# Performance work log

Measured on AMD Instinct MI355X. Metric: run time of the kernel, lower is better.

## Reference

```python
import jax, jax.numpy as jnp
import numpy as np

ORDER = 7
ALPHA = 1.0
BETA = 1.0

def _jacobi_coeffs(order, a, b):
    k1 = np.zeros(order + 1, dtype=np.float32)
    k2 = np.zeros(order + 1, dtype=np.float32)
    k3 = np.zeros(order + 1, dtype=np.float32)
    for i in range(2, order + 1):
        k1[i] = (2*i + a + b) * (2*i + a + b - 1) / (2*i * (i + a + b))
        k2[i] = (2*i + a + b - 1) * (a*a - b*b) / (2*i * (i + a + b) * (2*i + a + b - 2))
        k3[i] = (i + a - 1) * (i + b - 1) * (2*i + a + b) / (i * (i + a + b) * (2*i + a + b - 2))
    return k1, k2, k3

K1, K2, K3 = _jacobi_coeffs(ORDER, ALPHA, BETA)

def setup_inputs() -> dict:
    key = jax.random.key(0)
    kx, kc = jax.random.split(key)
    batch, input_size, output_size = 4096, 512, 512
    x = jax.random.normal(kx, (batch, input_size), dtype=jnp.float32)
    coef = jax.random.normal(kc, (output_size, input_size, ORDER + 1), dtype=jnp.float32) * 0.1
    return {"x": x, "coef": coef}

def _precompute_jacobi(x):
    # x: [B, I] -> jacobi values [B, I, order+1]
    x = jnp.tanh(x)
    p0 = jnp.ones_like(x)
    p1 = 0.5 * (ALPHA + BETA + 2.0) * x - 0.5 * (ALPHA - BETA)
    vals = [p0, p1]
    for i in range(2, ORDER + 1):
        vals.append((K1[i] * x + K2[i]) * vals[i - 1] - K3[i] * vals[i - 2])
    return jnp.stack(vals, axis=2)  # [B, I, D]

def reference(x, coef):
    jac = _precompute_jacobi(x)                 # [B, I, D]
    # sum_j over input and order dims in one contraction
    return jnp.einsum('bid,jid->bj', jac, coef)  # [B, O]
```

## Files before the change

### kernel.cpp

```cpp
#include <hip/hip_runtime.h>
#include <stdint.h>

#define BATCH 4096
#define ISZ   512
#define OSZ   512
#define KDIM  4096

#define TM 128
#define TN 128
#define BK 64
#define SPLITK 4

typedef __bf16 bf16x8 __attribute__((ext_vector_type(8)));
typedef float  f32x4  __attribute__((ext_vector_type(4)));

__device__ __forceinline__ unsigned short f2bf(float f) {
    uint32_t u = __float_as_uint(f);
    u = (u + 0x7FFFu + ((u >> 16) & 1u)) >> 16;
    return (unsigned short)u;
}

__global__ __launch_bounds__(256) void convert_bf16(
    const float* __restrict__ src, unsigned short* __restrict__ dst, int n4)
{
    int idx = blockIdx.x * 256 + threadIdx.x;
    if (idx >= n4) return;
    float4 v = reinterpret_cast<const float4*>(src)[idx];
    uint2 o;
    o.x = (uint32_t)f2bf(v.x) | ((uint32_t)f2bf(v.y) << 16);
    o.y = (uint32_t)f2bf(v.z) | ((uint32_t)f2bf(v.w) << 16);
    reinterpret_cast<uint2*>(dst)[idx] = o;
}

__global__ __launch_bounds__(256, 2) void gemm_fused(
    const float* __restrict__ X,
    const unsigned short* __restrict__ Bm,
    unsigned short* __restrict__ Cp,
    int M, int N, int K)
{
    __shared__ __align__(16) unsigned short As[2][TM * BK];
    __shared__ __align__(16) unsigned short Bs[2][TN * BK];

    const int tid  = threadIdx.x;
    const int wave = tid >> 6;
    const int lane = tid & 63;
    const int wm   = (wave >> 1) * 64;
    const int wn   = (wave & 1) * 64;

    const int    m0    = blockIdx.x * TM;
    const size_t baseB = (size_t)blockIdx.y * TN * K;
    const int kper  = K / SPLITK;
    const int kbeg  = blockIdx.z * kper;
    const int niter = kper / BK;

    f32x4 acc[4][4] = {};

    const int mrow = lane & 15;
    const int kc   = lane >> 4;

    const int xr = tid >> 1;
    const int xc = (tid & 1) * 4;

    auto stageB = [&](int k0, int buf) {
        #pragma unroll
        for (int it = 0; it < 4; ++it) {
            int s    = it * 256 + tid;
            int row  = s >> 3;
            int csrc = (s & 7) ^ (row & 7);
            const unsigned short* gB = Bm + baseB + (size_t)row * K + k0 + csrc * 8;
            unsigned short* lB = &Bs[buf][0] + (size_t)(it * 256 + wave * 64) * 8;
            __builtin_amdgcn_global_load_lds(
                (const __attribute__((address_space(1))) uint32_t*)gB,
                (__attribute__((address_space(3))) uint32_t*)lB, 16, 0, 0);
        }
    };

    auto stageA = [&](int k0, int buf) {
        const int i0 = k0 >> 3;
        float4 xv = *reinterpret_cast<const float4*>(
            X + (size_t)(m0 + xr) * ISZ + i0 + xc);
        const float xs[4] = {xv.x, xv.y, xv.z, xv.w};
        #pragma unroll
        for (int j = 0; j < 4; ++j) {
            float e  = __expf(2.0f * xs[j]);
            float t  = 1.0f - 2.0f * __builtin_amdgcn_rcpf(e + 1.0f);
            float p0 = 1.0f;
            float p1 = 2.0f * t;
            float p2 = (1.875f     * t) * p1 - 0.75f       * p0;
            float p3 = (1.8666667f * t) * p2 - 0.8f        * p1;
            float p4 = (1.875f     * t) * p3 - 0.83333333f * p2;
            float p5 = (1.8857143f * t) * p4 - 0.85714287f * p3;
            float p6 = (1.8958333f * t) * p5 - 0.875f      * p4;
            float p7 = (1.9047619f * t) * p6 - 0.88888889f * p5;
            uint4 o;
            o.x = (uint32_t)f2bf(p0) | ((uint32_t)f2bf(p1) << 16);
            o.y = (uint32_t)f2bf(p2) | ((uint32_t)f2bf(p3) << 16);
            o.z = (uint32_t)f2bf(p4) | ((uint32_t)f2bf(p5) << 16);
            o.w = (uint32_t)f2bf(p6) | ((uint32_t)f2bf(p7) << 16);
            int slot = xr * 8 + ((xc + j) ^ (xr & 7));
            *reinterpret_cast<uint4*>(&As[buf][0] + (size_t)slot * 8) = o;
        }
    };

    stageB(kbeg, 0);
    stageA(kbeg, 0);
    __syncthreads();

    for (int kt = 0; kt < niter; ++kt) {
        const int k0 = kbeg + kt * BK;
        const int p  = kt & 1;
        if (kt + 1 < niter) {
            stageB(k0 + BK, 1 - p);
            stageA(k0 + BK, 1 - p);
        }

        const unsigned short* Ap = &As[p][0];
        const unsigned short* Bp = &Bs[p][0];
        #pragma unroll
        for (int ks = 0; ks < BK; ks += 32) {
            bf16x8 aF[4], bF[4];
            const int cbase = (ks >> 3) + kc;
            #pragma unroll
            for (int mi = 0; mi < 4; ++mi) {
                int r = wm + mi * 16 + mrow;
                int slot = r * 8 + (cbase ^ (r & 7));
                aF[mi] = *reinterpret_cast<const bf16x8*>(Ap + (size_t)slot * 8);
            }
            #pragma unroll
            for (int ni = 0; ni < 4; ++ni) {
                int r = wn + ni * 16 + mrow;
                int slot = r * 8 + (cbase ^ (r & 7));
                bF[ni] = *reinterpret_cast<const bf16x8*>(Bp + (size_t)slot * 8);
            }
            #pragma unroll
            for (int mi = 0; mi < 4; ++mi)
                #pragma unroll
                for (int ni = 0; ni < 4; ++ni)
                    acc[mi][ni] = __builtin_amdgcn_mfma_f32_16x16x32_bf16(
                        aF[mi], bF[ni], acc[mi][ni], 0, 0, 0);
        }
        __syncthreads();
    }

    unsigned short* Cz = Cp + (size_t)blockIdx.z * M * N;
    const int orow = blockIdx.x * TM + wm + (lane >> 4) * 4;
    const int ocol = blockIdx.y * TN + wn + (lane & 15);
    #pragma unroll
    for (int mi = 0; mi < 4; ++mi)
        #pragma unroll
        for (int ni = 0; ni < 4; ++ni)
            #pragma unroll
            for (int r = 0; r < 4; ++r)
                Cz[(size_t)(orow + mi * 16 + r) * N + ocol + ni * 16] =
                    f2bf(acc[mi][ni][r]);
}

__global__ __launch_bounds__(256) void reduce_k(
    const unsigned short* __restrict__ part, float* __restrict__ out, int n4)
{
    int idx = blockIdx.x * 256 + threadIdx.x;
    if (idx >= n4) return;
    const uint2* p = reinterpret_cast<const uint2*>(part);
    float s0 = 0.f, s1 = 0.f, s2 = 0.f, s3 = 0.f;
    #pragma unroll
    for (int z = 0; z < SPLITK; ++z) {
        uint2 v = p[(size_t)z * n4 + idx];
        s0 += __uint_as_float((v.x & 0xFFFFu) << 16);
        s1 += __uint_as_float(v.x & 0xFFFF0000u);
        s2 += __uint_as_float((v.y & 0xFFFFu) << 16);
        s3 += __uint_as_float(v.y & 0xFFFF0000u);
    }
    float4 o = {s0, s1, s2, s3};
    reinterpret_cast<float4*>(out)[idx] = o;
}

extern "C" void kernel_launch(void* const* d_in, const int* in_sizes, int n_in,
                              void* d_out, int out_size, void* d_ws, size_t ws_size,
                              hipStream_t stream)
{
    const float* x    = (const float*)d_in[0];
    const float* coef = (const float*)d_in[1];
    float* out = (float*)d_out;

    unsigned short* part  = (unsigned short*)d_ws;
    unsigned short* coefb = part + (size_t)SPLITK * BATCH * OSZ;

    int n4c = (OSZ * KDIM) / 4;
    convert_bf16<<<(n4c + 255) / 256, 256, 0, stream>>>(coef, coefb, n4c);

    dim3 grid(BATCH / TM, OSZ / TN, SPLITK);
    gemm_fused<<<grid, 256, 0, stream>>>(x, coefb, part, BATCH, OSZ, KDIM);

    int n4r = (BATCH * OSZ) / 4;
    reduce_k<<<(n4r + 255) / 256, 256, 0, stream>>>(part, out, n4r);
}
```

Before: 101.8 us.

## Precompute Jacobi basis into bf16 buffer and stream A via global_load_lds

Moves the tanh plus Jacobi recurrence out of the GEMM's A-staging path into a combined prep kernel that also converts coef to bf16. The GEMM now loads both A and B tiles asynchronously with global_load_lds instead of computing A in registers, so recomputation across the OSZ/TN column blocks goes away. The split-K reduce is widened to 8 elements per thread. In exchange it writes and rereads a 32 MB bf16 basis matrix, adding global memory traffic.

```diff
diff --git a/kernel.cpp b/kernel.cpp
--- a/kernel.cpp
+++ b/kernel.cpp
@@ -20,20 +20,44 @@
     return (unsigned short)u;
 }
 
-__global__ __launch_bounds__(256) void convert_bf16(
-    const float* __restrict__ src, unsigned short* __restrict__ dst, int n4)
+#define NB_CONV 2048
+#define NB_JAC  8192
+__global__ __launch_bounds__(256) void prep(
+    const float* __restrict__ coef, unsigned short* __restrict__ coefb,
+    const float* __restrict__ X,    unsigned short* __restrict__ Ab)
 {
-    int idx = blockIdx.x * 256 + threadIdx.x;
-    if (idx >= n4) return;
-    float4 v = reinterpret_cast<const float4*>(src)[idx];
-    uint2 o;
-    o.x = (uint32_t)f2bf(v.x) | ((uint32_t)f2bf(v.y) << 16);
-    o.y = (uint32_t)f2bf(v.z) | ((uint32_t)f2bf(v.w) << 16);
-    reinterpret_cast<uint2*>(dst)[idx] = o;
+    const int b = blockIdx.x;
+    if (b < NB_CONV) {
+        int idx = b * 256 + threadIdx.x;
+        float4 v = reinterpret_cast<const float4*>(coef)[idx];
+        uint2 o;
+        o.x = (uint32_t)f2bf(v.x) | ((uint32_t)f2bf(v.y) << 16);
+        o.y = (uint32_t)f2bf(v.z) | ((uint32_t)f2bf(v.w) << 16);
+        reinterpret_cast<uint2*>(coefb)[idx] = o;
+    } else {
+        int idx = (b - NB_CONV) * 256 + threadIdx.x;
+        float x = X[idx];
+        float e  = __expf(2.0f * x);
+        float t  = 1.0f - 2.0f * __builtin_amdgcn_rcpf(e + 1.0f);
+        float p0 = 1.0f;
+        float p1 = 2.0f * t;
+        float p2 = (1.875f     * t) * p1 - 0.75f       * p0;
+        float p3 = (1.8666667f * t) * p2 - 0.8f        * p1;
+        float p4 = (1.875f     * t) * p3 - 0.83333333f * p2;
+        float p5 = (1.8857143f * t) * p4 - 0.85714287f * p3;
+        float p6 = (1.8958333f * t) * p5 - 0.875f      * p4;
+        float p7 = (1.9047619f * t) * p6 - 0.88888889f * p5;
+        uint4 o;
+        o.x = (uint32_t)f2bf(p0) | ((uint32_t)f2bf(p1) << 16);
+        o.y = (uint32_t)f2bf(p2) | ((uint32_t)f2bf(p3) << 16);
+        o.z = (uint32_t)f2bf(p4) | ((uint32_t)f2bf(p5) << 16);
+        o.w = (uint32_t)f2bf(p6) | ((uint32_t)f2bf(p7) << 16);
+        reinterpret_cast<uint4*>(Ab)[idx] = o;
+    }
 }
 
 __global__ __launch_bounds__(256, 2) void gemm_fused(
-    const float* __restrict__ X,
+    const unsigned short* __restrict__ Am,
     const unsigned short* __restrict__ Bm,
     unsigned short* __restrict__ Cp,
     int M, int N, int K)
@@ -47,7 +71,7 @@
     const int wm   = (wave >> 1) * 64;
     const int wn   = (wave & 1) * 64;
 
-    const int    m0    = blockIdx.x * TM;
+    const size_t baseA = (size_t)blockIdx.x * TM * K;
     const size_t baseB = (size_t)blockIdx.y * TN * K;
     const int kper  = K / SPLITK;
     const int kbeg  = blockIdx.z * kper;
@@ -58,60 +82,31 @@
     const int mrow = lane & 15;
     const int kc   = lane >> 4;
 
-    const int xr = tid >> 1;
-    const int xc = (tid & 1) * 4;
-
-    auto stageB = [&](int k0, int buf) {
+    auto stage = [&](const unsigned short* __restrict__ G, size_t gbase,
+                     unsigned short* lds, int k0) {
         #pragma unroll
         for (int it = 0; it < 4; ++it) {
             int s    = it * 256 + tid;
             int row  = s >> 3;
             int csrc = (s & 7) ^ (row & 7);
-            const unsigned short* gB = Bm + baseB + (size_t)row * K + k0 + csrc * 8;
-            unsigned short* lB = &Bs[buf][0] + (size_t)(it * 256 + wave * 64) * 8;
+            const unsigned short* g = G + gbase + (size_t)row * K + k0 + csrc * 8;
+            unsigned short* l = lds + (size_t)(it * 256 + wave * 64) * 8;
             __builtin_amdgcn_global_load_lds(
-                (const __attribute__((address_space(1))) uint32_t*)gB,
-                (__attribute__((address_space(3))) uint32_t*)lB, 16, 0, 0);
+                (const __attribute__((address_space(1))) uint32_t*)g,
+                (__attribute__((address_space(3))) uint32_t*)l, 16, 0, 0);
         }
     };
 
-    auto stageA = [&](int k0, int buf) {
-        const int i0 = k0 >> 3;
-        float4 xv = *reinterpret_cast<const float4*>(
-            X + (size_t)(m0 + xr) * ISZ + i0 + xc);
-        const float xs[4] = {xv.x, xv.y, xv.z, xv.w};
-        #pragma unroll
-        for (int j = 0; j < 4; ++j) {
-            float e  = __expf(2.0f * xs[j]);
-            float t  = 1.0f - 2.0f * __builtin_amdgcn_rcpf(e + 1.0f);
-            float p0 = 1.0f;
-            float p1 = 2.0f * t;
-            float p2 = (1.875f     * t) * p1 - 0.75f       * p0;
-            float p3 = (1.8666667f * t) * p2 - 0.8f        * p1;
-            float p4 = (1.875f     * t) * p3 - 0.83333333f * p2;
-            float p5 = (1.8857143f * t) * p4 - 0.85714287f * p3;
-            float p6 = (1.8958333f * t) * p5 - 0.875f      * p4;
-            float p7 = (1.9047619f * t) * p6 - 0.88888889f * p5;
-            uint4 o;
-            o.x = (uint32_t)f2bf(p0) | ((uint32_t)f2bf(p1) << 16);
-            o.y = (uint32_t)f2bf(p2) | ((uint32_t)f2bf(p3) << 16);
-            o.z = (uint32_t)f2bf(p4) | ((uint32_t)f2bf(p5) << 16);
-            o.w = (uint32_t)f2bf(p6) | ((uint32_t)f2bf(p7) << 16);
-            int slot = xr * 8 + ((xc + j) ^ (xr & 7));
-            *reinterpret_cast<uint4*>(&As[buf][0] + (size_t)slot * 8) = o;
-        }
-    };
-
-    stageB(kbeg, 0);
-    stageA(kbeg, 0);
+    stage(Bm, baseB, &Bs[0][0], kbeg);
+    stage(Am, baseA, &As[0][0], kbeg);
     __syncthreads();
 
     for (int kt = 0; kt < niter; ++kt) {
         const int k0 = kbeg + kt * BK;
         const int p  = kt & 1;
         if (kt + 1 < niter) {
-            stageB(k0 + BK, 1 - p);
-            stageA(k0 + BK, 1 - p);
+            stage(Bm, baseB, &Bs[1 - p][0], k0 + BK);
+            stage(Am, baseA, &As[1 - p][0], k0 + BK);
         }
 
         const unsigned short* Ap = &As[p][0];
@@ -156,22 +151,28 @@
 }
 
 __global__ __launch_bounds__(256) void reduce_k(
-    const unsigned short* __restrict__ part, float* __restrict__ out, int n4)
+    const unsigned short* __restrict__ part, float* __restrict__ out, int n8)
 {
     int idx = blockIdx.x * 256 + threadIdx.x;
-    if (idx >= n4) return;
-    const uint2* p = reinterpret_cast<const uint2*>(part);
-    float s0 = 0.f, s1 = 0.f, s2 = 0.f, s3 = 0.f;
+    if (idx >= n8) return;
+    const uint4* p = reinterpret_cast<const uint4*>(part);
+    float s[8] = {};
     #pragma unroll
     for (int z = 0; z < SPLITK; ++z) {
-        uint2 v = p[(size_t)z * n4 + idx];
-        s0 += __uint_as_float((v.x & 0xFFFFu) << 16);
-        s1 += __uint_as_float(v.x & 0xFFFF0000u);
-        s2 += __uint_as_float((v.y & 0xFFFFu) << 16);
-        s3 += __uint_as_float(v.y & 0xFFFF0000u);
+        uint4 v = p[(size_t)z * n8 + idx];
+        s[0] += __uint_as_float((v.x & 0xFFFFu) << 16);
+        s[1] += __uint_as_float(v.x & 0xFFFF0000u);
+        s[2] += __uint_as_float((v.y & 0xFFFFu) << 16);
+        s[3] += __uint_as_float(v.y & 0xFFFF0000u);
+        s[4] += __uint_as_float((v.z & 0xFFFFu) << 16);
+        s[5] += __uint_as_float(v.z & 0xFFFF0000u);
+        s[6] += __uint_as_float((v.w & 0xFFFFu) << 16);
+        s[7] += __uint_as_float(v.w & 0xFFFF0000u);
     }
-    float4 o = {s0, s1, s2, s3};
-    reinterpret_cast<float4*>(out)[idx] = o;
+    float4 o0 = {s[0], s[1], s[2], s[3]};
+    float4 o1 = {s[4], s[5], s[6], s[7]};
+    reinterpret_cast<float4*>(out)[2 * idx]     = o0;
+    reinterpret_cast<float4*>(out)[2 * idx + 1] = o1;
 }
 
 extern "C" void kernel_launch(void* const* d_in, const int* in_sizes, int n_in,
@@ -183,14 +184,14 @@
     float* out = (float*)d_out;
 
     unsigned short* part  = (unsigned short*)d_ws;
-    unsigned short* coefb = part + (size_t)SPLITK * BATCH * OSZ;
+    unsigned short* coefb = part  + (size_t)SPLITK * BATCH * OSZ;
+    unsigned short* Ab    = coefb + (size_t)OSZ * KDIM;
 
-    int n4c = (OSZ * KDIM) / 4;
-    convert_bf16<<<(n4c + 255) / 256, 256, 0, stream>>>(coef, coefb, n4c);
+    prep<<<NB_CONV + NB_JAC, 256, 0, stream>>>(coef, coefb, x, Ab);
 
     dim3 grid(BATCH / TM, OSZ / TN, SPLITK);
-    gemm_fused<<<grid, 256, 0, stream>>>(x, coefb, part, BATCH, OSZ, KDIM);
+    gemm_fused<<<grid, 256, 0, stream>>>(Ab, coefb, part, BATCH, OSZ, KDIM);
 
-    int n4r = (BATCH * OSZ) / 4;
-    reduce_k<<<(n4r + 255) / 256, 256, 0, stream>>>(part, out, n4r);
+    int n8r = (BATCH * OSZ) / 8;
+    reduce_k<<<(n8r + 255) / 256, 256, 0, stream>>>(part, out, n8r);
 }
```

Measured after the change: 96.02 us. -5.7%, faster.
